# Kernel tuning notes

Measured on AMD Instinct MI355X. Metric: run time of the kernel, lower is better.

## Reference

```python
import jax, jax.numpy as jnp
import numpy as np

B, T = 64, 512          # batch, seq_len
D = 512                 # model_size / LSTM hidden
V = 256                 # vocab_size
R, W, M = 4, 16, 5      # read_heads, cell_size, nr_cells
RW = R * W
IFC = R * W + 3 * W + 5 * R + 3   # DNC interface vector size = 135
EPS = 1e-6
CLIP = 20.0


def setup_inputs():
    ks = jax.random.split(jax.random.key(0), 12)
    s = 0.05
    f32 = jnp.float32
    return {
        'tokens':   jax.random.randint(ks[0], (B, T), 0, V, dtype=jnp.int32),
        'emb':      jax.random.normal(ks[1], (V, D), f32),
        'lstm_Wi0': jax.random.normal(ks[2], (4 * D, D + RW), f32) * s,
        'lstm_Wh0': jax.random.normal(ks[3], (4 * D, D), f32) * s,
        'lstm_b0':  jnp.zeros((4 * D,), f32),
        'lstm_Wi1': jax.random.normal(ks[4], (4 * D, D), f32) * s,
        'lstm_Wh1': jax.random.normal(ks[5], (4 * D, D), f32) * s,
        'lstm_b1':  jnp.zeros((4 * D,), f32),
        'W_if':     jax.random.normal(ks[6], (IFC, D), f32) * s,
        'b_if':     jnp.zeros((IFC,), f32),
        'W_out':    jax.random.normal(ks[7], (D, D + RW), f32) * s,
        'b_out':    jnp.zeros((D,), f32),
        'W_fc':     jax.random.normal(ks[8], (V, D), f32) * s,
        'b_fc':     jnp.zeros((V,), f32),
    }


def _cosine(mem, keys):
    # mem (B,M,W), keys (B,K,W) -> (B,K,M) batchwise cosine similarity
    mn = mem / (jnp.linalg.norm(mem, axis=2, keepdims=True) + EPS)
    kn = keys / (jnp.linalg.norm(keys, axis=2, keepdims=True) + EPS)
    return jnp.einsum('bkw,bmw->bkm', kn, mn)


def _allocate(usage):
    # DNC allocation weighting via sort + exclusive cumprod, then unsort
    u = EPS + (1.0 - EPS) * usage                           # (B,M)
    idx = jnp.argsort(u, axis=1)                            # ascending usage
    sorted_u = jnp.take_along_axis(u, idx, axis=1)
    prod_excl = jnp.cumprod(
        jnp.concatenate([jnp.ones_like(u[:, :1]), sorted_u], axis=1), axis=1)[:, :-1]
    alloc_sorted = (1.0 - sorted_u) * prod_excl
    inv = jnp.argsort(idx, axis=1)                          # reverse permutation
    return jnp.take_along_axis(alloc_sorted, inv, axis=1)


def _dnc_forward(tokens, emb, lstm_Wi0, lstm_Wh0, lstm_b0,
                 lstm_Wi1, lstm_Wh1, lstm_b1, W_if, b_if,
                 W_out, b_out, W_fc, b_fc):
    x = emb[tokens]                                         # (B,T,D)
    eye_mask = 1.0 - jnp.eye(M, dtype=x.dtype)

    def lstm_cell(xin, h, c, Wi, Wh, b):
        g = xin @ Wi.T + h @ Wh.T + b
        i, f, gg, o = jnp.split(g, 4, axis=1)               # torch gate order i,f,g,o
        c2 = jax.nn.sigmoid(f) * c + jax.nn.sigmoid(i) * jnp.tanh(gg)
        h2 = jax.nn.sigmoid(o) * jnp.tanh(c2)
        return h2, c2

    def step(carry, x_t):
        h0, c0, h1, c1, mem, link, prec, rw_p, ww_p, usage, last_read = carry
        xin = jnp.concatenate([x_t, last_read], axis=1)     # (B, D+RW)
        nh0, nc0 = lstm_cell(xin, h0, c0, lstm_Wi0, lstm_Wh0, lstm_b0)
        nh1, nc1 = lstm_cell(nh0, h1, c1, lstm_Wi1, lstm_Wh1, lstm_b1)
        out = jnp.clip(nh1, -CLIP, CLIP)
        xi = out @ W_if.T + b_if                            # (B, IFC)

        o = 0
        read_keys = jnp.tanh(xi[:, :RW]).reshape(-1, R, W); o = RW
        read_str  = jax.nn.softplus(xi[:, o:o + R]); o += R
        write_key = jnp.tanh(xi[:, o:o + W]); o += W
        write_str = jax.nn.softplus(xi[:, o]); o += 1
        erase     = jax.nn.sigmoid(xi[:, o:o + W]); o += W
        write_vec = jnp.tanh(xi[:, o:o + W]); o += W
        free_g    = jax.nn.sigmoid(xi[:, o:o + R]); o += R
        alloc_g   = jax.nn.sigmoid(xi[:, o]); o += 1
        write_g   = jax.nn.sigmoid(xi[:, o]); o += 1
        read_modes = jax.nn.softmax(xi[:, o:o + 3 * R].reshape(-1, R, 3), axis=-1)

        # ---- write head ----
        usage2 = usage + (1.0 - usage) * ww_p               # single write head
        psi = jnp.prod(1.0 - free_g[:, :, None] * rw_p, axis=1)   # (B,M)
        usage2 = usage2 * psi
        wcw = jax.nn.softmax(
            _cosine(mem, write_key[:, None, :])[:, 0, :] * write_str[:, None], axis=1)
        alloc = _allocate(usage2)
        ww = write_g[:, None] * (alloc_g[:, None] * alloc
                                 + (1.0 - alloc_g[:, None]) * wcw)  # (B,M)
        mem2 = mem * (1.0 - ww[:, :, None] * erase[:, None, :]) \
               + ww[:, :, None] * write_vec[:, None, :]
        link2 = (1.0 - ww[:, :, None] - ww[:, None, :]) * link \
                + ww[:, :, None] * prec[:, None, :]
        link2 = link2 * eye_mask
        prec2 = (1.0 - jnp.sum(ww, axis=1, keepdims=True)) * prec + ww

        # ---- read heads ----
        rcw = jax.nn.softmax(_cosine(mem2, read_keys) * read_str[:, :, None], axis=2)
        fwd = jnp.einsum('bij,brj->bri', link2, rw_p)       # L @ w_prev
        bwd = jnp.einsum('bij,bri->brj', link2, rw_p)       # L^T @ w_prev
        rw = (read_modes[..., 0:1] * bwd + read_modes[..., 1:2] * fwd
              + read_modes[..., 2:3] * rcw)                 # (B,R,M)
        read_vecs = jnp.einsum('brm,bmw->brw', rw, mem2).reshape(-1, RW)

        y = jnp.concatenate([out, read_vecs], axis=1) @ W_out.T + b_out  # (B,D)
        carry = (nh0, nc0, nh1, nc1, mem2, link2, prec2, rw, ww, usage2, read_vecs)
        return carry, y

    b = tokens.shape[0]
    z = lambda *shape: jnp.zeros(shape, x.dtype)
    carry0 = (z(b, D), z(b, D), z(b, D), z(b, D),
              z(b, M, W), z(b, M, M), z(b, M),
              z(b, R, M), z(b, M), z(b, M), z(b, RW))
    _, ys = jax.lax.scan(step, carry0, jnp.swapaxes(x, 0, 1))
    y = jnp.swapaxes(ys, 0, 1)                              # (B,T,D)
    logits = y @ W_fc.T + b_fc                              # (B,T,V)
    return jnp.transpose(logits, (0, 2, 1))                 # (B,V,T)


def reference(tokens, emb, lstm_Wi0, lstm_Wh0, lstm_b0,
              lstm_Wi1, lstm_Wh1, lstm_b1, W_if, b_if,
              W_out, b_out, W_fc, b_fc):
    return _dnc_forward(tokens, emb, lstm_Wi0, lstm_Wh0, lstm_b0,
                        lstm_Wi1, lstm_Wh1, lstm_b1, W_if, b_if,
                        W_out, b_out, W_fc, b_fc)
```

## Files before the change

kernel.cpp:

```cpp
#include <hip/hip_runtime.h>
#include <hip/hip_bf16.h>

typedef __hip_bfloat16 bf16;
typedef _Float16 f16;
typedef _Float16 f16x8 __attribute__((ext_vector_type(8)));
typedef float f32x4 __attribute__((ext_vector_type(4)));
typedef unsigned long long u64;
typedef unsigned short ushort_t;

__device__ __forceinline__ float b2f(bf16 x){ return __bfloat162float(x); }
__device__ __forceinline__ float sigf(float x){ return 1.f/(1.f+expf(-x)); }
__device__ __forceinline__ float splus(float x){ return fmaxf(x,0.f)+log1pf(expf(-fabsf(x))); }
__device__ __forceinline__ float ldf(const void* p, int i, int isf32){
  return isf32 ? ((const float*)p)[i] : __bfloat162float(((const bf16*)p)[i]);
}
__device__ __forceinline__ void ast64(u64* p, u64 v){ __hip_atomic_store(p, v, __ATOMIC_RELAXED, __HIP_MEMORY_SCOPE_AGENT); }
__device__ __forceinline__ u64 ald64(u64* p){ return __hip_atomic_load(p, __ATOMIC_RELAXED, __HIP_MEMORY_SCOPE_AGENT); }
__device__ __forceinline__ void ast32(unsigned* p, unsigned v){ __hip_atomic_store(p, v, __ATOMIC_RELAXED, __HIP_MEMORY_SCOPE_AGENT); }
__device__ __forceinline__ unsigned ald32(unsigned* p){ return __hip_atomic_load(p, __ATOMIC_RELAXED, __HIP_MEMORY_SCOPE_AGENT); }

union U4H8 { uint4 u; f16x8 h; };
union U64H4 { u64 u; f16 h[4]; };
union H16 { f16 h; ushort_t s; };

__global__ void k_detect(const void* __restrict__ emb, int* __restrict__ flag){
  __shared__ float mx[256];
  int tid=threadIdx.x;
  float v = fabsf(__bfloat162float(((const bf16*)emb)[tid]));
  mx[tid]=v; __syncthreads();
  for(int s=128;s>0;s>>=1){ if(tid<s) mx[tid]=fmaxf(mx[tid],mx[tid+s]); __syncthreads(); }
  if(tid==0){ flag[0] = (mx[0]>1000.f) ? 1 : 0; flag[1] = 0; }
}

__global__ void k_embW(const void* __restrict__ emb, const void* __restrict__ Wi0,
                       const void* __restrict__ b0,
                       const int* __restrict__ flags, float* __restrict__ embW){
  int f=flags[0];
  int row = blockIdx.x;
  __shared__ float w[512];
  for(int k=threadIdx.x;k<512;k+=256) w[k]=ldf(Wi0,row*576+k,f);
  __syncthreads();
  int v = threadIdx.x;
  float acc=ldf(b0,row,f);
  #pragma unroll 4
  for(int k=0;k<512;k++) acc += ldf(emb,v*512+k,f)*w[k];
  embW[row*256+v]=acc;
}

__global__ void k_wpkA(const void* __restrict__ Wh0, const void* __restrict__ Wi0,
                       const int* __restrict__ flags, ushort_t* __restrict__ PA){
  int f=flags[0];
  int idx=blockIdx.x*256+threadIdx.x;
  if(idx>=1179648) return;
  int j=idx&7, l=(idx>>3)&63, rest=idx>>9;
  int c=rest%18, t2=rest/18, w=t2&7, r=t2>>3;
  int tr=l&15, q4=l>>4;
  int G=tr&3, dd=tr>>2;
  int row=G*512 + r*32 + w*4 + dd;
  int k=c*32 + q4*8 + j;
  float val = (k<512)? ldf(Wh0,row*512+k,f) : ldf(Wi0,row*576+k,f);
  H16 hx; hx.h=(f16)val; PA[idx]=hx.s;
}
__global__ void k_wpkB(const void* __restrict__ Wi1, const void* __restrict__ Wh1,
                       const int* __restrict__ flags, ushort_t* __restrict__ PB){
  int f=flags[0];
  int idx=blockIdx.x*256+threadIdx.x;
  if(idx>=2097152) return;
  int j=idx&7, l=(idx>>3)&63, rest=idx>>9;
  int c=rest&31, t2=rest>>5, w=t2&7, r=t2>>3;
  int tr=l&15, q4=l>>4;
  int G=tr&3, dd=tr>>2;
  int row=G*512 + r*32 + w*4 + dd;
  int k=c*32 + q4*8 + j;
  float val = (k<512)? ldf(Wi1,row*512+k,f) : ldf(Wh1,row*512+k-512,f);
  H16 hx; hx.h=(f16)val; PB[idx]=hx.s;
}

__global__ void k_wifP(const void* __restrict__ W_if, const void* __restrict__ b_if,
                       const int* __restrict__ flags,
                       ushort_t* __restrict__ PW, float* __restrict__ b_ifF,
                       unsigned* __restrict__ FLz){
  int f=flags[0];
  int idx=blockIdx.x*256+threadIdx.x;
  if(idx<73728){
    int j=idx&7, l=(idx>>3)&63, c=(idx>>9)&15, tile=idx>>13;
    int row=tile*16+(l&15);
    int k=c*32+(l>>4)*8+j;
    float val=(row<135)? ldf(W_if,row*512+k,f) : 0.f;
    H16 hx; hx.h=(f16)val; PW[idx]=hx.s;
  }
  if(idx<64) FLz[idx]=0u;
  if(idx<135) b_ifF[idx]=ldf(b_if,idx,f);
}

__global__ void k_wc(const void* __restrict__ W_fc, const void* __restrict__ W_out,
                     const void* __restrict__ b_out, const void* __restrict__ b_fc,
                     const int* __restrict__ flags,
                     float* __restrict__ Wc, float* __restrict__ bc){
  int f=flags[0];
  int idx=blockIdx.x*256+threadIdx.x;
  int v=idx/576, j=idx-v*576;
  float acc=0.f;
  #pragma unroll 4
  for(int d=0;d<512;d++) acc += ldf(W_fc,v*512+d,f)*ldf(W_out,d*576+j,f);
  Wc[idx]=acc;
  if(j==0){
    float a=ldf(b_fc,v,f);
    for(int d=0;d<512;d++) a += ldf(W_fc,v*512+d,f)*ldf(b_out,d,f);
    bc[v]=a;
  }
}

__global__ void __launch_bounds__(512, 2) k_dnc3(
    const int* __restrict__ tokens, const void* __restrict__ b1, const int* __restrict__ flags,
    const float* __restrict__ embW, const ushort_t* __restrict__ PA, const ushort_t* __restrict__ PB,
    const ushort_t* __restrict__ PW, const float* __restrict__ b_ifF,
    u64* GX0, u64* GX1, unsigned* FL,
    bf16* __restrict__ cat)
{
  const int bid = blockIdx.x;
  const int g   = bid>>4, r = bid&15;
  const int tid = threadIdx.x;
  const int wv  = tid>>6, l = tid&63;
  const int lm  = l&15,  q4 = l>>4;
  const int mb  = tid>>5, mu = tid&31;
  const int f32i = flags[0];

  __shared__ __align__(16) u64 HB[4352];
  __shared__ f16  sh_pub[512];
  __shared__ int  tokL[16];
  __shared__ float b_ifL[144];
  __shared__ float xis2[16*149];
  __shared__ float s_pre[16*112];
  __shared__ float s_mem[1280], s_mem2[1280], s_link[400], s_link2[400];
  __shared__ float s_prec[80], s_prec2[80], s_rwp[320], s_rw[320];
  __shared__ float s_wwp[80], s_ww[80], s_usage[80], s_wl[80];
  __shared__ float s_rl[320], s_fwd[320], s_bwd[320], s_wsum[16];
  __shared__ float rvbuf[1024];

#define WAITG(TGT) do{ if(tid<16){ unsigned _tg=(unsigned)(TGT); int _wd=0; \
    while(ald32(&FL[g*16+tid]) < _tg && _wd<50000000){ __builtin_amdgcn_s_sleep(1); _wd++; } } \
  __syncthreads(); }while(0)
#define PUBF(VAL) do{ __syncthreads(); \
  if(tid==0) ast32(&FL[g*16+r],(unsigned)(VAL)); }while(0)
#define XI(i) xis2[mb*149+(i)]
#define WB() __builtin_amdgcn_wave_barrier()

  const f16x8* HBv=(const f16x8*)HB;
  const uint4* PAv=(const uint4*)PA;
  const uint4* PBv=(const uint4*)PB;
  const uint4* PWv=(const uint4*)PW;

  const int dim1 = r*32 + wv*4 + q4;
  const float b1Li=ldf(b1,dim1,f32i), b1Lf=ldf(b1,512+dim1,f32i),
              b1Lg=ldf(b1,1024+dim1,f32i), b1Lo=ldf(b1,1536+dim1,f32i);

  if(tid<144) b_ifL[tid]=(tid<135)? b_ifF[tid] : 0.f;
  for(int i=tid;i<1280;i+=512) s_mem[i]=0.f;
  for(int i=tid;i<400;i+=512) s_link[i]=0.f;
  for(int i=tid;i<320;i+=512) s_rwp[i]=0.f;
  if(tid<80){ s_prec[tid]=0.f; s_wwp[tid]=0.f; s_usage[tid]=0.f; }
  float c0s=0.f, c1s=0.f;

  if(tid<16) tokL[tid]=tokens[(g*16+tid)*512];
  __syncthreads();
  {
    int tok=tokL[lm];
    float ei=embW[dim1*256+tok];
    float eg=embW[262144+dim1*256+tok];
    float eo=embW[393216+dim1*256+tok];
    c0s = sigf(ei)*tanhf(eg);
    sh_pub[(wv*4+q4)*16+lm]=(f16)(sigf(eo)*tanhf(c0s));
  }
  __syncthreads();
  if(tid<128){
    int ks=tid>>4, b2=tid&15;
    U64H4 pk;
    #pragma unroll
    for(int i=0;i<4;i++) pk.h[i]=sh_pub[(ks*4+i)*16+b2];
    ast64(&GX0[g*4096+((4*r+(ks>>1))*16+b2)*2+(ks&1)], pk.u);
  }
  PUBF(2u);
  WAITG(2u);
  {
    u64 s0=ald64(&GX0[g*4096+tid      ]);
    u64 s1=ald64(&GX0[g*4096+tid+512  ]);
    u64 s2=ald64(&GX0[g*4096+tid+1024 ]);
    u64 s3=ald64(&GX0[g*4096+tid+1536 ]);
    HB[tid]=s0; HB[tid+512]=s1; HB[tid+1024]=s2; HB[tid+1536]=s3;
  }
  __syncthreads();
  {
    f32x4 acc1=(f32x4){0.f,0.f,0.f,0.f};
    #pragma unroll
    for(int c=0;c<16;c++){
      U4H8 wf; wf.u=PBv[((r*8+wv)*32+c)*64+l];
      f16x8 bfr=HBv[(c*4+q4)*16+lm];
      acc1=__builtin_amdgcn_mfma_f32_16x16x32_f16(wf.h,bfr,acc1,0,0,0);
    }
    float gi=acc1[0]+b1Li, gg=acc1[2]+b1Lg, go=acc1[3]+b1Lo;
    c1s=sigf(gi)*tanhf(gg);
    sh_pub[(wv*4+q4)*16+lm]=(f16)(sigf(go)*tanhf(c1s));
  }
  __syncthreads();
  if(tid<128){
    int ks=tid>>4, b2=tid&15;
    U64H4 pk;
    #pragma unroll
    for(int i=0;i<4;i++) pk.h[i]=sh_pub[(ks*4+i)*16+b2];
    ast64(&GX1[g*4096+((4*r+(ks>>1))*16+b2)*2+(ks&1)], pk.u);
  }
  PUBF(3u);

  for(int tt=0;tt<512;tt++){
    const int p=tt&1, pn=p^1;

    f32x4 accA=(f32x4){0.f,0.f,0.f,0.f};
    #pragma unroll
    for(int c=0;c<16;c++){
      U4H8 wf; wf.u=PAv[((r*8+wv)*18+c)*64+l];
      f16x8 bfr=HBv[(c*4+q4)*16+lm];
      accA=__builtin_amdgcn_mfma_f32_16x16x32_f16(wf.h,bfr,accA,0,0,0);
    }
    float em0,em1,em2,em3;
    {
      int tn=(tt<511)?tt+1:511;
      int tok=tokens[(g*16+lm)*512+tn];
      em0=embW[dim1*256+tok]; em1=embW[131072+dim1*256+tok];
      em2=embW[262144+dim1*256+tok]; em3=embW[393216+dim1*256+tok];
    }
    uint4 pfA2[2];
    #pragma unroll
    for(int c2=0;c2<2;c2++) pfA2[c2]=PAv[((r*8+wv)*18+16+c2)*64+l];
    uint4 pfP3[16];
    #pragma unroll
    for(int cc=0;cc<16;cc++) pfP3[cc]=PWv[(wv*16+cc)*64+l];

    WAITG(2*tt+3);

    {
      u64 s0=ald64(&GX1[g*4096+p*2048+tid      ]);
      u64 s1=ald64(&GX1[g*4096+p*2048+tid+512  ]);
      u64 s2=ald64(&GX1[g*4096+p*2048+tid+1024 ]);
      u64 s3=ald64(&GX1[g*4096+p*2048+tid+1536 ]);
      HB[2048+tid]=s0; HB[2048+tid+512]=s1; HB[2048+tid+1024]=s2; HB[2048+tid+1536]=s3;
    }
    __syncthreads();

    {
      f32x4 xa=(f32x4){0.f,0.f,0.f,0.f};
      #pragma unroll
      for(int cc=0;cc<16;cc++){
        U4H8 t4; t4.u=pfP3[cc];
        f16x8 bfr=HBv[1024+(cc*4+q4)*16+lm];
        xa=__builtin_amdgcn_mfma_f32_16x16x32_f16(t4.h,bfr,xa,0,0,0);
      }
      #pragma unroll
      for(int reg=0;reg<4;reg++){
        int row=wv*16+q4*4+reg;
        xis2[lm*149+row]=xa[reg]+b_ifL[row];
      }
      if(wv==0){
        f32x4 xb=(f32x4){0.f,0.f,0.f,0.f};
        #pragma unroll
        for(int cc=0;cc<16;cc++){
          U4H8 t4; t4.u=PWv[(128+cc)*64+l];
          f16x8 bfr=HBv[1024+(cc*4+q4)*16+lm];
          xb=__builtin_amdgcn_mfma_f32_16x16x32_f16(t4.h,bfr,xb,0,0,0);
        }
        #pragma unroll
        for(int reg=0;reg<4;reg++){
          int row=128+q4*4+reg;
          xis2[lm*149+row]=xb[reg]+b_ifL[row];
        }
      }
    }
    __syncthreads();

    if(mu<16){
      s_pre[mb*112+mu]    =tanhf(XI(68+mu));
      s_pre[mb*112+16+mu] =sigf (XI(85+mu));
      s_pre[mb*112+32+mu] =tanhf(XI(101+mu));
    }
    s_pre[mb*112+48+mu]   =tanhf(XI(mu));
    s_pre[mb*112+48+32+mu]=tanhf(XI(32+mu));
    WB();
    if(mu<5){
      int m=mu;
      float u=s_usage[mb*5+m]+(1.f-s_usage[mb*5+m])*s_wwp[mb*5+m];
      float psi=1.f;
      #pragma unroll
      for(int rr=0;rr<4;rr++) psi *= 1.f - sigf(XI(117+rr))*s_rwp[mb*20+rr*5+m];
      u*=psi; s_usage[mb*5+m]=u;
      float nm=0.f,dt=0.f,nk=0.f;
      #pragma unroll
      for(int w=0;w<16;w++){
        float mv=s_mem[mb*80+m*16+w], kv=s_pre[mb*112+w];
        nm+=mv*mv; dt+=mv*kv; nk+=kv*kv;
      }
      float sim=dt/((sqrtf(nm)+1e-6f)*(sqrtf(nk)+1e-6f));
      s_wl[mb*5+m]=sim*splus(XI(84));
    }
    WB();
    if(mu<5){
      int m=mu;
      float mx=s_wl[mb*5];
      #pragma unroll
      for(int j=1;j<5;j++) mx=fmaxf(mx,s_wl[mb*5+j]);
      float e=expf(s_wl[mb*5+m]-mx);
      float u=1e-6f+(1.f-1e-6f)*s_usage[mb*5+m];
      s_rl [mb*20+m]=u;
      s_bwd[mb*20+m]=e;
    }
    WB();
    if(mu<5){
      int m=mu;
      float u=s_rl[mb*20+m], e=s_bwd[mb*20+m];
      float s=0.f, prod=1.f;
      #pragma unroll
      for(int j=0;j<5;j++){
        s+=s_bwd[mb*20+j];
        float uj=s_rl[mb*20+j];
        if(uj<u || (uj==u && j<m)) prod*=uj;
      }
      float wcw=e/s;
      float alloc=(1.f-u)*prod;
      float ag=sigf(XI(121)), wgg=sigf(XI(122));
      s_ww[mb*5+m]=wgg*(ag*alloc+(1.f-ag)*wcw);
    }
    WB();
    if(mu==0){
      float ws=0.f;
      #pragma unroll
      for(int m=0;m<5;m++) ws+=s_ww[mb*5+m];
      s_wsum[mb]=ws;
    }
    WB();
    for(int k=mu;k<80;k+=32){
      int m=k>>4,w=k&15;
      float er=s_pre[mb*112+16+w], wv2=s_pre[mb*112+32+w];
      float w_=s_ww[mb*5+m];
      s_mem2[mb*80+k]=s_mem[mb*80+k]*(1.f-w_*er)+w_*wv2;
    }
    if(mu<25){
      int i=mu/5, j=mu-5*i;
      s_link2[mb*25+mu]=(i==j)?0.f:((1.f-s_ww[mb*5+i]-s_ww[mb*5+j])*s_link[mb*25+mu]+s_ww[mb*5+i]*s_prec[mb*5+j]);
    } else if(mu<30){
      int j=mu-25;
      s_prec2[mb*5+j]=(1.f-s_wsum[mb])*s_prec[mb*5+j]+s_ww[mb*5+j];
    }
    WB();
    if(mu<20){
      int rr=mu/5, m=mu-5*rr;
      float nm=0.f,dt=0.f,nk=0.f;
      #pragma unroll
      for(int w=0;w<16;w++){
        float mv=s_mem2[mb*80+m*16+w], kv=s_pre[mb*112+48+rr*16+w];
        nm+=mv*mv; dt+=mv*kv; nk+=kv*kv;
      }
      float sim=dt/((sqrtf(nm)+1e-6f)*(sqrtf(nk)+1e-6f));
      s_rl[mb*20+mu]=sim*splus(XI(64+rr));
      float af=0.f, ab=0.f;
      #pragma unroll
      for(int j=0;j<5;j++) af+=s_link2[mb*25+m*5+j]*s_rwp[mb*20+rr*5+j];
      #pragma unroll
      for(int i=0;i<5;i++) ab+=s_link2[mb*25+i*5+m]*s_rwp[mb*20+rr*5+i];
      s_fwd[mb*20+rr*5+m]=af;
      s_bwd[mb*20+rr*5+m]=ab;
    }
    WB();
    if(mu<20){
      int rr=mu/5;
      float mx=-1e30f;
      #pragma unroll
      for(int m=0;m<5;m++) mx=fmaxf(mx,s_rl[mb*20+rr*5+m]);
      float s=0.f;
      #pragma unroll
      for(int m=0;m<5;m++) s+=expf(s_rl[mb*20+rr*5+m]-mx);
      float rcw=expf(s_rl[mb*20+mu]-mx)/s;
      float q0=XI(123+3*rr),q1=XI(124+3*rr),q2=XI(125+3*rr);
      float m3=fmaxf(q0,fmaxf(q1,q2));
      float e0=expf(q0-m3),e1=expf(q1-m3),e2=expf(q2-m3);
      float inv=1.f/(e0+e1+e2);
      s_rw[mb*20+mu]=(e0*s_bwd[mb*20+mu]+e1*s_fwd[mb*20+mu]+e2*rcw)*inv;
    }
    WB();
    for(int k=mu;k<64;k+=32){
      int rr=k>>4,w=k&15;
      float a=0.f;
      #pragma unroll
      for(int m=0;m<5;m++) a+=s_rw[mb*20+rr*5+m]*s_mem2[mb*80+m*16+w];
      rvbuf[mb*64+k]=a;
    }
    for(int k=mu;k<80;k+=32) s_mem[mb*80+k]=s_mem2[mb*80+k];
    if(mu<25) s_link[mb*25+mu]=s_link2[mb*25+mu];
    else if(mu<30) s_prec[mb*5+mu-25]=s_prec2[mb*5+mu-25];
    if(mu<20) s_rwp[mb*20+mu]=s_rw[mb*20+mu];
    if(mu>=27&&mu<32){ int m=mu-27; s_wwp[mb*5+m]=s_ww[mb*5+m]; }
    __syncthreads();

    if(tt==511){
      int cb=((g*16+r)*512+tt)*576;
      if(tid<128){
        int kg=tid>>1, e=tid&1;
        U64H4 pv; pv.u=HB[2048+(kg*16+r)*2+e];
        #pragma unroll
        for(int i=0;i<4;i++){
          float x=(float)pv.h[i];
          cat[cb+kg*8+e*4+i]=__float2bfloat16(fminf(fmaxf(x,-20.f),20.f));
        }
      }
      if(tid<64) cat[cb+512+tid]=__float2bfloat16(rvbuf[r*64+tid]);
      break;
    }

    if(tid<256){
      int kg=tid>>5, rem=tid&31, b2=rem>>1, e=rem&1;
      U64H4 pk;
      #pragma unroll
      for(int i=0;i<4;i++) pk.h[i]=(f16)rvbuf[b2*64 + kg*8+e*4+i];
      HB[4096+(kg*16+b2)*2+e]=pk.u;
    }
    __syncthreads();
    #pragma unroll
    for(int c2=0;c2<2;c2++){
      U4H8 wf; wf.u=pfA2[c2];
      f16x8 bfr=HBv[2048+(c2*4+q4)*16+lm];
      accA=__builtin_amdgcn_mfma_f32_16x16x32_f16(wf.h,bfr,accA,0,0,0);
    }
    {
      float gi=accA[0]+em0, gf=accA[1]+em1, gg=accA[2]+em2, go=accA[3]+em3;
      float c0=sigf(gf)*c0s+sigf(gi)*tanhf(gg);
      c0s=c0;
      sh_pub[(wv*4+q4)*16+lm]=(f16)(sigf(go)*tanhf(c0));
    }
    __syncthreads();
    if(tid<128){
      int ks=tid>>4, b2=tid&15;
      U64H4 pk;
      #pragma unroll
      for(int i=0;i<4;i++) pk.h[i]=sh_pub[(ks*4+i)*16+b2];
      ast64(&GX0[g*4096+pn*2048+((4*r+(ks>>1))*16+b2)*2+(ks&1)], pk.u);
    }
    PUBF(2*tt+4);

    f32x4 accB=(f32x4){0.f,0.f,0.f,0.f};
    #pragma unroll
    for(int c=16;c<32;c++){
      U4H8 wf; wf.u=PBv[((r*8+wv)*32+c)*64+l];
      f16x8 bfr=HBv[1024+((c-16)*4+q4)*16+lm];
      accB=__builtin_amdgcn_mfma_f32_16x16x32_f16(wf.h,bfr,accB,0,0,0);
    }
    uint4 pfB2[16];
    #pragma unroll
    for(int c=0;c<16;c++) pfB2[c]=PBv[((r*8+wv)*32+c)*64+l];
    {
      int cb=((g*16+r)*512+tt)*576;
      if(tid<128){
        int kg=tid>>1, e=tid&1;
        U64H4 pv; pv.u=HB[2048+(kg*16+r)*2+e];
        #pragma unroll
        for(int i=0;i<4;i++){
          float x=(float)pv.h[i];
          cat[cb+kg*8+e*4+i]=__float2bfloat16(fminf(fmaxf(x,-20.f),20.f));
        }
      }
      if(tid<64) cat[cb+512+tid]=__float2bfloat16(rvbuf[r*64+tid]);
    }

    WAITG(2*tt+4);

    {
      u64 s0=ald64(&GX0[g*4096+pn*2048+tid      ]);
      u64 s1=ald64(&GX0[g*4096+pn*2048+tid+512  ]);
      u64 s2=ald64(&GX0[g*4096+pn*2048+tid+1024 ]);
      u64 s3=ald64(&GX0[g*4096+pn*2048+tid+1536 ]);
      HB[tid]=s0; HB[tid+512]=s1; HB[tid+1024]=s2; HB[tid+1536]=s3;
    }
    __syncthreads();
    #pragma unroll
    for(int c=0;c<16;c++){
      U4H8 wf; wf.u=pfB2[c];
      f16x8 bfr=HBv[(c*4+q4)*16+lm];
      accB=__builtin_amdgcn_mfma_f32_16x16x32_f16(wf.h,bfr,accB,0,0,0);
    }
    {
      float gi=accB[0]+b1Li, gf=accB[1]+b1Lf, gg=accB[2]+b1Lg, go=accB[3]+b1Lo;
      float c1=sigf(gf)*c1s+sigf(gi)*tanhf(gg);
      c1s=c1;
      sh_pub[(wv*4+q4)*16+lm]=(f16)(sigf(go)*tanhf(c1));
    }
    __syncthreads();
    if(tid<128){
      int ks=tid>>4, b2=tid&15;
      U64H4 pk;
      #pragma unroll
      for(int i=0;i<4;i++) pk.h[i]=sh_pub[(ks*4+i)*16+b2];
      ast64(&GX1[g*4096+pn*2048+((4*r+(ks>>1))*16+b2)*2+(ks&1)], pk.u);
    }
    PUBF(2*tt+5);
  }
#undef WAITG
#undef PUBF
#undef XI
#undef WB
}

__global__ void __launch_bounds__(256) k_out(const bf16* __restrict__ cat,
                                             const float* __restrict__ Wc,
                                             const float* __restrict__ bc,
                                             float* __restrict__ outp){
  int t0=blockIdx.x*64, v0=blockIdx.y*64, b=blockIdx.z;
  __shared__ float As[64][33];
  __shared__ float Bs[32][65];
  int tid=threadIdx.x;
  int ti=tid>>4, vi=tid&15;
  float acc[4][4]={};
  for(int k0=0;k0<576;k0+=32){
    for(int i=tid;i<64*32;i+=256){
      int rr=i>>5,k=i&31;
      As[rr][k]=b2f(cat[(b*512+t0+rr)*576+k0+k]);
    }
    for(int i=tid;i<64*32;i+=256){
      int v=i>>5,k=i&31;
      Bs[k][v]=Wc[(v0+v)*576+k0+k];
    }
    __syncthreads();
    #pragma unroll 8
    for(int kk=0;kk<32;kk++){
      float av[4],bv[4];
      #pragma unroll
      for(int x=0;x<4;x++) av[x]=As[ti*4+x][kk];
      #pragma unroll
      for(int y=0;y<4;y++) bv[y]=Bs[kk][vi*4+y];
      #pragma unroll
      for(int x=0;x<4;x++)
        #pragma unroll
        for(int y=0;y<4;y++) acc[x][y]+=av[x]*bv[y];
    }
    __syncthreads();
  }
  #pragma unroll
  for(int y=0;y<4;y++){
    int v=v0+vi*4+y;
    float bcv=bc[v];
    #pragma unroll
    for(int x=0;x<4;x++){
      int tt=t0+ti*4+x;
      outp[(b*256+v)*512+tt]=acc[x][y]+bcv;
    }
  }
}

extern "C" void kernel_launch(void* const* d_in, const int* in_sizes, int n_in,
                              void* d_out, int out_size, void* d_ws, size_t ws_size,
                              hipStream_t stream) {
  const int*  tokens = (const int*) d_in[0];
  const void* emb    = d_in[1];
  const void* Wi0    = d_in[2];
  const void* Wh0    = d_in[3];
  const void* b0     = d_in[4];
  const void* Wi1    = d_in[5];
  const void* Wh1    = d_in[6];
  const void* b1     = d_in[7];
  const void* W_if   = d_in[8];
  const void* b_if   = d_in[9];
  const void* W_out  = d_in[10];
  const void* b_out  = d_in[11];
  const void* W_fc   = d_in[12];
  const void* b_fc   = d_in[13];

  static const int expect[14] = {64*512, 256*512, 2048*576, 2048*512, 2048,
                                 2048*512, 2048*512, 2048, 135*512, 135,
                                 512*576, 512, 256*512, 256};
  bool ok = (n_in == 14);
  if(ok) for(int i=0;i<14;i++) if(in_sizes[i]!=expect[i]) ok=false;

  int*      flags = (int*)d_ws;
  float*    embW  = (float*)d_ws + 64;
  ushort_t* PA    = (ushort_t*)(embW + 524288);
  ushort_t* PB    = PA + 1310720;
  float*    Wreg  = (float*)(PB + 2097152);
  float*    b_ifF = Wreg + 69632;
  float*    Wc    = b_ifF + 160;
  float*    bc    = Wc + 147456;
  u64*      GX0   = (u64*)(bc + 256);
  u64*      GX1   = GX0 + 16384;
  u64*      GXL   = GX1 + 16384;
  bf16*     cat   = (bf16*)(GXL + 2048);
  unsigned* FL    = (unsigned*)(PA + 1179648);
  ushort_t* PW    = (ushort_t*)Wreg;

  size_t need = 9783168ull + 278528ull + 37748736ull;
  if(!ok || ws_size < need){
    hipMemsetAsync(d_out, 0, (size_t)out_size*4, stream);
    return;
  }

  k_detect<<<dim3(1), dim3(256), 0, stream>>>(emb, flags);
  k_embW<<<dim3(2048), dim3(256), 0, stream>>>(emb, Wi0, b0, flags, embW);
  k_wpkA<<<dim3(4608), dim3(256), 0, stream>>>(Wh0, Wi0, flags, PA);
  k_wpkB<<<dim3(8192), dim3(256), 0, stream>>>(Wi1, Wh1, flags, PB);
  k_wifP<<<dim3(288), dim3(256), 0, stream>>>(W_if, b_if, flags, PW, b_ifF, FL);
  k_wc  <<<dim3(576),  dim3(256), 0, stream>>>(W_fc, W_out, b_out, b_fc, flags, Wc, bc);

  void* kargs[] = {
    (void*)&tokens, (void*)&b1, (void*)&flags,
    (void*)&embW, (void*)&PA, (void*)&PB,
    (void*)&PW, (void*)&b_ifF,
    (void*)&GX0, (void*)&GX1, (void*)&FL,
    (void*)&cat
  };
  hipLaunchCooperativeKernel((const void*)k_dnc3, dim3(64), dim3(512), kargs, 0, stream);

  k_out<<<dim3(8,4,64), dim3(256), 0, stream>>>(cat, Wc, bc, (float*)d_out);
}
```

Measured before the change: 11.75 ms.

## Tile weight-precompute GEMMs in shared memory and split MFMA accumulator chains

Rewrites the embedding-projection and fused output-weight precompute kernels as 64x64 shared-memory tiled GEMMs with 4x4 register blocking. The old versions used one thread per output with poor data reuse. The recurrent kernel's MFMA reductions now alternate between two independent accumulators, which shortens the dependent MFMA chain in each timestep. This costs a few extra registers and one vector add per gate computation, and the summation order changes slightly.

After: 11.27 ms. 1.04x faster.

```diff
diff --git a/kernel.cpp b/kernel.cpp
--- a/kernel.cpp
+++ b/kernel.cpp
@@ -32,19 +32,47 @@
   if(tid==0){ flag[0] = (mx[0]>1000.f) ? 1 : 0; flag[1] = 0; }
 }
 
-__global__ void k_embW(const void* __restrict__ emb, const void* __restrict__ Wi0,
+__global__ void __launch_bounds__(256) k_embW(const void* __restrict__ emb, const void* __restrict__ Wi0,
                        const void* __restrict__ b0,
                        const int* __restrict__ flags, float* __restrict__ embW){
   int f=flags[0];
-  int row = blockIdx.x;
-  __shared__ float w[512];
-  for(int k=threadIdx.x;k<512;k+=256) w[k]=ldf(Wi0,row*576+k,f);
-  __syncthreads();
-  int v = threadIdx.x;
-  float acc=ldf(b0,row,f);
-  #pragma unroll 4
-  for(int k=0;k<512;k++) acc += ldf(emb,v*512+k,f)*w[k];
-  embW[row*256+v]=acc;
+  int r0=blockIdx.x*64, v0=blockIdx.y*64;
+  __shared__ float As[64][33];
+  __shared__ float Bs[32][65];
+  int tid=threadIdx.x;
+  int ti=tid>>4, vi=tid&15;
+  float acc[4][4]={};
+  for(int k0=0;k0<512;k0+=32){
+    for(int i=tid;i<64*32;i+=256){
+      int rr=i>>5,k=i&31;
+      As[rr][k]=ldf(Wi0,(r0+rr)*576+k0+k,f);
+    }
+    for(int i=tid;i<64*32;i+=256){
+      int v=i>>5,k=i&31;
+      Bs[k][v]=ldf(emb,(v0+v)*512+k0+k,f);
+    }
+    __syncthreads();
+    #pragma unroll 8
+    for(int kk=0;kk<32;kk++){
+      float av[4],bv[4];
+      #pragma unroll
+      for(int x=0;x<4;x++) av[x]=As[ti*4+x][kk];
+      #pragma unroll
+      for(int y=0;y<4;y++) bv[y]=Bs[kk][vi*4+y];
+      #pragma unroll
+      for(int x=0;x<4;x++)
+        #pragma unroll
+        for(int y=0;y<4;y++) acc[x][y]+=av[x]*bv[y];
+    }
+    __syncthreads();
+  }
+  #pragma unroll
+  for(int x=0;x<4;x++){
+    int row=r0+ti*4+x;
+    float b=ldf(b0,row,f);
+    #pragma unroll
+    for(int y=0;y<4;y++) embW[row*256+v0+vi*4+y]=acc[x][y]+b;
+  }
 }
 
 __global__ void k_wpkA(const void* __restrict__ Wh0, const void* __restrict__ Wi0,
@@ -93,21 +121,55 @@
   if(idx<135) b_ifF[idx]=ldf(b_if,idx,f);
 }
 
-__global__ void k_wc(const void* __restrict__ W_fc, const void* __restrict__ W_out,
+__global__ void __launch_bounds__(256) k_wc(const void* __restrict__ W_fc, const void* __restrict__ W_out,
                      const void* __restrict__ b_out, const void* __restrict__ b_fc,
                      const int* __restrict__ flags,
                      float* __restrict__ Wc, float* __restrict__ bc){
   int f=flags[0];
-  int idx=blockIdx.x*256+threadIdx.x;
-  int v=idx/576, j=idx-v*576;
-  float acc=0.f;
-  #pragma unroll 4
-  for(int d=0;d<512;d++) acc += ldf(W_fc,v*512+d,f)*ldf(W_out,d*576+j,f);
-  Wc[idx]=acc;
-  if(j==0){
-    float a=ldf(b_fc,v,f);
-    for(int d=0;d<512;d++) a += ldf(W_fc,v*512+d,f)*ldf(b_out,d,f);
-    bc[v]=a;
+  int v0=blockIdx.x*64, j0=blockIdx.y*64;
+  __shared__ float As[64][33];
+  __shared__ float Bs[32][65];
+  __shared__ float red[64][4];
+  int tid=threadIdx.x;
+  int ti=tid>>4, vi=tid&15;
+  float acc[4][4]={};
+  for(int k0=0;k0<512;k0+=32){
+    for(int i=tid;i<64*32;i+=256){
+      int vv=i>>5,k=i&31;
+      As[vv][k]=ldf(W_fc,(v0+vv)*512+k0+k,f);
+    }
+    for(int i=tid;i<64*32;i+=256){
+      int jj=i>>5,k=i&31;
+      Bs[k][jj]=ldf(W_out,(k0+k)*576+j0+jj,f);
+    }
+    __syncthreads();
+    #pragma unroll 8
+    for(int kk=0;kk<32;kk++){
+      float av[4],bv[4];
+      #pragma unroll
+      for(int x=0;x<4;x++) av[x]=As[ti*4+x][kk];
+      #pragma unroll
+      for(int y=0;y<4;y++) bv[y]=Bs[kk][vi*4+y];
+      #pragma unroll
+      for(int x=0;x<4;x++)
+        #pragma unroll
+        for(int y=0;y<4;y++) acc[x][y]+=av[x]*bv[y];
+    }
+    __syncthreads();
+  }
+  #pragma unroll
+  for(int x=0;x<4;x++){
+    int v=v0+ti*4+x;
+    #pragma unroll
+    for(int y=0;y<4;y++) Wc[v*576+j0+vi*4+y]=acc[x][y];
+  }
+  if(blockIdx.y==0){
+    int v=tid>>2, pp=tid&3;
+    float a=0.f;
+    for(int d=pp*128;d<pp*128+128;d++) a+=ldf(W_fc,(v0+v)*512+d,f)*ldf(b_out,d,f);
+    red[v][pp]=a;
+    __syncthreads();
+    if(pp==0) bc[v0+v]=ldf(b_fc,v0+v,f)+red[v][0]+red[v][1]+red[v][2]+red[v][3];
   }
 }
 
@@ -215,12 +277,16 @@
   for(int tt=0;tt<512;tt++){
     const int p=tt&1, pn=p^1;
 
-    f32x4 accA=(f32x4){0.f,0.f,0.f,0.f};
-    #pragma unroll
-    for(int c=0;c<16;c++){
-      U4H8 wf; wf.u=PAv[((r*8+wv)*18+c)*64+l];
-      f16x8 bfr=HBv[(c*4+q4)*16+lm];
-      accA=__builtin_amdgcn_mfma_f32_16x16x32_f16(wf.h,bfr,accA,0,0,0);
+    f32x4 accA0=(f32x4){0.f,0.f,0.f,0.f};
+    f32x4 accA1=(f32x4){0.f,0.f,0.f,0.f};
+    #pragma unroll
+    for(int c=0;c<16;c+=2){
+      U4H8 wf0; wf0.u=PAv[((r*8+wv)*18+c)*64+l];
+      f16x8 bf0=HBv[(c*4+q4)*16+lm];
+      accA0=__builtin_amdgcn_mfma_f32_16x16x32_f16(wf0.h,bf0,accA0,0,0,0);
+      U4H8 wf1; wf1.u=PAv[((r*8+wv)*18+c+1)*64+l];
+      f16x8 bf1=HBv[((c+1)*4+q4)*16+lm];
+      accA1=__builtin_amdgcn_mfma_f32_16x16x32_f16(wf1.h,bf1,accA1,0,0,0);
     }
     float em0,em1,em2,em3;
     {
@@ -248,26 +314,36 @@
     __syncthreads();
 
     {
-      f32x4 xa=(f32x4){0.f,0.f,0.f,0.f};
-      #pragma unroll
-      for(int cc=0;cc<16;cc++){
-        U4H8 t4; t4.u=pfP3[cc];
-        f16x8 bfr=HBv[1024+(cc*4+q4)*16+lm];
-        xa=__builtin_amdgcn_mfma_f32_16x16x32_f16(t4.h,bfr,xa,0,0,0);
+      f32x4 xa0=(f32x4){0.f,0.f,0.f,0.f};
+      f32x4 xa1=(f32x4){0.f,0.f,0.f,0.f};
+      #pragma unroll
+      for(int cc=0;cc<16;cc+=2){
+        U4H8 t0; t0.u=pfP3[cc];
+        f16x8 bf0=HBv[1024+(cc*4+q4)*16+lm];
+        xa0=__builtin_amdgcn_mfma_f32_16x16x32_f16(t0.h,bf0,xa0,0,0,0);
+        U4H8 t1; t1.u=pfP3[cc+1];
+        f16x8 bf1=HBv[1024+((cc+1)*4+q4)*16+lm];
+        xa1=__builtin_amdgcn_mfma_f32_16x16x32_f16(t1.h,bf1,xa1,0,0,0);
       }
+      f32x4 xa=xa0+xa1;
       #pragma unroll
       for(int reg=0;reg<4;reg++){
         int row=wv*16+q4*4+reg;
         xis2[lm*149+row]=xa[reg]+b_ifL[row];
       }
       if(wv==0){
-        f32x4 xb=(f32x4){0.f,0.f,0.f,0.f};
+        f32x4 xb0=(f32x4){0.f,0.f,0.f,0.f};
+        f32x4 xb1=(f32x4){0.f,0.f,0.f,0.f};
         #pragma unroll
-        for(int cc=0;cc<16;cc++){
-          U4H8 t4; t4.u=PWv[(128+cc)*64+l];
-          f16x8 bfr=HBv[1024+(cc*4+q4)*16+lm];
-          xb=__builtin_amdgcn_mfma_f32_16x16x32_f16(t4.h,bfr,xb,0,0,0);
+        for(int cc=0;cc<16;cc+=2){
+          U4H8 t0; t0.u=PWv[(128+cc)*64+l];
+          f16x8 bf0=HBv[1024+(cc*4+q4)*16+lm];
+          xb0=__builtin_amdgcn_mfma_f32_16x16x32_f16(t0.h,bf0,xb0,0,0,0);
+          U4H8 t1; t1.u=PWv[(128+cc+1)*64+l];
+          f16x8 bf1=HBv[1024+((cc+1)*4+q4)*16+lm];
+          xb1=__builtin_amdgcn_mfma_f32_16x16x32_f16(t1.h,bf1,xb1,0,0,0);
         }
+        f32x4 xb=xb0+xb1;
         #pragma unroll
         for(int reg=0;reg<4;reg++){
           int row=128+q4*4+reg;
@@ -422,13 +498,16 @@
       HB[4096+(kg*16+b2)*2+e]=pk.u;
     }
     __syncthreads();
-    #pragma unroll
-    for(int c2=0;c2<2;c2++){
-      U4H8 wf; wf.u=pfA2[c2];
-      f16x8 bfr=HBv[2048+(c2*4+q4)*16+lm];
-      accA=__builtin_amdgcn_mfma_f32_16x16x32_f16(wf.h,bfr,accA,0,0,0);
-    }
     {
+      U4H8 wf0; wf0.u=pfA2[0];
+      f16x8 bf0=HBv[2048+(0*4+q4)*16+lm];
+      accA0=__builtin_amdgcn_mfma_f32_16x16x32_f16(wf0.h,bf0,accA0,0,0,0);
+      U4H8 wf1; wf1.u=pfA2[1];
+      f16x8 bf1=HBv[2048+(1*4+q4)*16+lm];
+      accA1=__builtin_amdgcn_mfma_f32_16x16x32_f16(wf1.h,bf1,accA1,0,0,0);
+    }
+    {
+      f32x4 accA=accA0+accA1;
       float gi=accA[0]+em0, gf=accA[1]+em1, gg=accA[2]+em2, go=accA[3]+em3;
       float c0=sigf(gf)*c0s+sigf(gi)*tanhf(gg);
       c0s=c0;
@@ -444,12 +523,16 @@
     }
     PUBF(2*tt+4);
 
-    f32x4 accB=(f32x4){0.f,0.f,0.f,0.f};
-    #pragma unroll
-    for(int c=16;c<32;c++){
-      U4H8 wf; wf.u=PBv[((r*8+wv)*32+c)*64+l];
-      f16x8 bfr=HBv[1024+((c-16)*4+q4)*16+lm];
-      accB=__builtin_amdgcn_mfma_f32_16x16x32_f16(wf.h,bfr,accB,0,0,0);
+    f32x4 accB0=(f32x4){0.f,0.f,0.f,0.f};
+    f32x4 accB1=(f32x4){0.f,0.f,0.f,0.f};
+    #pragma unroll
+    for(int c=16;c<32;c+=2){
+      U4H8 wf0; wf0.u=PBv[((r*8+wv)*32+c)*64+l];
+      f16x8 bf0=HBv[1024+((c-16)*4+q4)*16+lm];
+      accB0=__builtin_amdgcn_mfma_f32_16x16x32_f16(wf0.h,bf0,accB0,0,0,0);
+      U4H8 wf1; wf1.u=PBv[((r*8+wv)*32+c+1)*64+l];
+      f16x8 bf1=HBv[1024+((c-15)*4+q4)*16+lm];
+      accB1=__builtin_amdgcn_mfma_f32_16x16x32_f16(wf1.h,bf1,accB1,0,0,0);
     }
     uint4 pfB2[16];
     #pragma unroll
@@ -479,12 +562,16 @@
     }
     __syncthreads();
     #pragma unroll
-    for(int c=0;c<16;c++){
-      U4H8 wf; wf.u=pfB2[c];
-      f16x8 bfr=HBv[(c*4+q4)*16+lm];
-      accB=__builtin_amdgcn_mfma_f32_16x16x32_f16(wf.h,bfr,accB,0,0,0);
+    for(int c=0;c<16;c+=2){
+      U4H8 wf0; wf0.u=pfB2[c];
+      f16x8 bf0=HBv[(c*4+q4)*16+lm];
+      accB0=__builtin_amdgcn_mfma_f32_16x16x32_f16(wf0.h,bf0,accB0,0,0,0);
+      U4H8 wf1; wf1.u=pfB2[c+1];
+      f16x8 bf1=HBv[((c+1)*4+q4)*16+lm];
+      accB1=__builtin_amdgcn_mfma_f32_16x16x32_f16(wf1.h,bf1,accB1,0,0,0);
     }
     {
+      f32x4 accB=accB0+accB1;
       float gi=accB[0]+b1Li, gf=accB[1]+b1Lf, gg=accB[2]+b1Lg, go=accB[3]+b1Lo;
       float c1=sigf(gf)*c1s+sigf(gi)*tanhf(gg);
       c1s=c1;
@@ -598,11 +685,11 @@
   }
 
   k_detect<<<dim3(1), dim3(256), 0, stream>>>(emb, flags);
-  k_embW<<<dim3(2048), dim3(256), 0, stream>>>(emb, Wi0, b0, flags, embW);
+  k_embW<<<dim3(32,4), dim3(256), 0, stream>>>(emb, Wi0, b0, flags, embW);
   k_wpkA<<<dim3(4608), dim3(256), 0, stream>>>(Wh0, Wi0, flags, PA);
   k_wpkB<<<dim3(8192), dim3(256), 0, stream>>>(Wi1, Wh1, flags, PB);
   k_wifP<<<dim3(288), dim3(256), 0, stream>>>(W_if, b_if, flags, PW, b_ifF, FL);
-  k_wc  <<<dim3(576),  dim3(256), 0, stream>>>(W_fc, W_out, b_out, b_fc, flags, Wc, bc);
+  k_wc  <<<dim3(4,9),  dim3(256), 0, stream>>>(W_fc, W_out, b_out, b_fc, flags, Wc, bc);
 
   void* kargs[] = {
     (void*)&tokens, (void*)&b1, (void*)&flags,
```
